# Kernel optimization log

Hardware: AMD Instinct MI355X
Metric: run time of the kernel (lower is better)

Reference implementation:

```python
import jax, jax.numpy as jnp
import numpy as np

MIN_BOX_SIZE = 0.05


def setup_inputs() -> dict:
    key = jax.random.key(0)
    mask_fg = jax.random.uniform(key, (256, 1, 512, 512), dtype=jnp.float32)
    return {"mask_fg": mask_fg}


def reference(mask_fg):
    # mask_fg: (B, 1, H, W). Returns boxes: (B, 4) as [x0, y0, x1, y1] in [0, 1].
    B, _, H, W = mask_fg.shape
    m = mask_fg[:, 0] > 0.5  # (B, H, W) boolean foreground mask

    row_any = jnp.any(m, axis=2)  # (B, H): row contains a foreground pixel
    col_any = jnp.any(m, axis=1)  # (B, W): col contains a foreground pixel
    empty = ~jnp.any(row_any, axis=1)  # (B,): no foreground at all

    ys = jnp.arange(H, dtype=jnp.float32)
    xs = jnp.arange(W, dtype=jnp.float32)

    # masked min/max of row / column indices, normalized (matches torch: idx / H, idx / W)
    y_min = jnp.min(jnp.where(row_any, ys, jnp.float32(H)), axis=1) / H
    y_max = jnp.max(jnp.where(row_any, ys, jnp.float32(-1)), axis=1) / H
    x_min = jnp.min(jnp.where(col_any, xs, jnp.float32(W)), axis=1) / W
    x_max = jnp.max(jnp.where(col_any, xs, jnp.float32(-1)), axis=1) / W

    s = jnp.float32(MIN_BOX_SIZE)

    def expand(lo, hi):
        too_small = (hi - lo) < s
        c = (lo + hi) * 0.5
        lo2 = jnp.maximum(jnp.float32(0.0), c - s * 0.5)
        hi2 = jnp.minimum(jnp.float32(1.0), c + s * 0.5)
        return jnp.where(too_small, lo2, lo), jnp.where(too_small, hi2, hi)

    x_min, x_max = expand(x_min, x_max)
    y_min, y_max = expand(y_min, y_max)

    boxes = jnp.stack([x_min, y_min, x_max, y_max], axis=1)  # (B, 4)
    default = jnp.array([0.25, 0.25, 0.75, 0.75], dtype=jnp.float32)
    boxes = jnp.where(empty[:, None], default[None, :], boxes)
    return boxes
```

## Files before the change

kernel.cpp:

```cpp
#include <hip/hip_runtime.h>


constexpr int H = 512;
constexpr int W = 512;
constexpr int THREADS = 512;
constexpr int NWAVE = THREADS / 64;
constexpr int BIG = 1 << 29;

__device__ __forceinline__ int block_min(int v, int t, int* s_tmp, int* s_res) {
    #pragma unroll
    for (int off = 32; off > 0; off >>= 1) v = min(v, __shfl_down(v, off));
    if ((t & 63) == 0) s_tmp[t >> 6] = v;
    __syncthreads();
    if (t == 0) {
        int m = s_tmp[0];
        #pragma unroll
        for (int w = 1; w < NWAVE; ++w) m = min(m, s_tmp[w]);
        *s_res = m;
    }
    __syncthreads();
    return *s_res;
}

__global__ __launch_bounds__(THREADS)
void scan_kernel(const float* __restrict__ mask, int* __restrict__ ws) {
    const int b = blockIdx.x;
    const int phase = blockIdx.y;
    const float4* __restrict__ img =
        reinterpret_cast<const float4*>(mask) + (size_t)b * (H * W / 4);
    const int t = threadIdx.x;
    __shared__ int s_tmp[NWAVE];
    __shared__ int s_res;

    int result = BIG;

    if (phase < 2) {
        const int rr = t >> 7;
        const int c4 = t & 127;
        for (int g = 0; g < H / 4; ++g) {
            const int gg = (phase == 0) ? g : (H / 4 - 1 - g);
            const int r = gg * 4 + rr;
            const float4 v = img[(r << 7) + c4];
            const bool fg = (v.x > 0.5f) || (v.y > 0.5f) ||
                            (v.z > 0.5f) || (v.w > 0.5f);
            const int key = fg ? (phase == 0 ? r : -r) : BIG;
            const int res = block_min(key, t, s_tmp, &s_res);
            if (res < BIG) { result = res; break; }
        }
    } else {
        const int r = t;
        for (int s = 0; s < W / 4; ++s) {
            const int ss = (phase == 2) ? s : (W / 4 - 1 - s);
            const float4 v = img[(r << 7) + ss];
            const int c = ss * 4;
            int key = BIG;
            if (phase == 2) {
                if (v.w > 0.5f) key = c + 3;
                if (v.z > 0.5f) key = c + 2;
                if (v.y > 0.5f) key = c + 1;
                if (v.x > 0.5f) key = c;
            } else {
                if (v.x > 0.5f) key = -c;
                if (v.y > 0.5f) key = -(c + 1);
                if (v.z > 0.5f) key = -(c + 2);
                if (v.w > 0.5f) key = -(c + 3);
            }
            const int res = block_min(key, t, s_tmp, &s_res);
            if (res < BIG) { result = res; break; }
        }
    }

    if (t == 0) ws[b * 4 + phase] = result;
}

__global__ __launch_bounds__(256)
void box_kernel(const int* __restrict__ ws, float* __restrict__ out, int B) {
    const int b = blockIdx.x * blockDim.x + threadIdx.x;
    if (b >= B) return;
    const int ymin = ws[b * 4 + 0];
    const int nymax = ws[b * 4 + 1];
    const int xmin = ws[b * 4 + 2];
    const int nxmax = ws[b * 4 + 3];
    float x0, y0, x1, y1;
    if (ymin >= BIG) {
        x0 = 0.25f; y0 = 0.25f; x1 = 0.75f; y1 = 0.75f;
    } else {
        const int ymax = -nymax, xmax = -nxmax;
        y0 = (float)ymin * (1.0f / H);
        y1 = (float)ymax * (1.0f / H);
        x0 = (float)xmin * (1.0f / W);
        x1 = (float)xmax * (1.0f / W);
        const float s = 0.05f;
        if (x1 - x0 < s) {
            const float c = (x0 + x1) * 0.5f;
            x0 = fmaxf(0.0f, c - s * 0.5f);
            x1 = fminf(1.0f, c + s * 0.5f);
        }
        if (y1 - y0 < s) {
            const float c = (y0 + y1) * 0.5f;
            y0 = fmaxf(0.0f, c - s * 0.5f);
            y1 = fminf(1.0f, c + s * 0.5f);
        }
    }
    reinterpret_cast<float4*>(out)[b] = make_float4(x0, y0, x1, y1);
}

extern "C" void kernel_launch(void* const* d_in, const int* in_sizes, int n_in,
                              void* d_out, int out_size, void* d_ws, size_t ws_size,
                              hipStream_t stream) {
    const float* mask = (const float*)d_in[0];
    float* out = (float*)d_out;
    int* ws = (int*)d_ws;
    const int B = in_sizes[0] / (H * W);
    dim3 grid(B, 4);
    scan_kernel<<<grid, THREADS, 0, stream>>>(mask, ws);
    box_kernel<<<(B + 255) / 256, 256, 0, stream>>>(ws, out, B);
}
```

Before: 301.9 us.

## Fuse scan and box kernels into one block per image with wave-level early exit

```diff
diff --git a/kernel.cpp b/kernel.cpp
--- a/kernel.cpp
+++ b/kernel.cpp
@@ -3,106 +3,94 @@
 
 constexpr int H = 512;
 constexpr int W = 512;
-constexpr int THREADS = 512;
-constexpr int NWAVE = THREADS / 64;
 constexpr int BIG = 1 << 29;
 
-__device__ __forceinline__ int block_min(int v, int t, int* s_tmp, int* s_res) {
+__device__ __forceinline__ int wave_min_bcast(int v) {
     #pragma unroll
     for (int off = 32; off > 0; off >>= 1) v = min(v, __shfl_down(v, off));
-    if ((t & 63) == 0) s_tmp[t >> 6] = v;
-    __syncthreads();
-    if (t == 0) {
-        int m = s_tmp[0];
-        #pragma unroll
-        for (int w = 1; w < NWAVE; ++w) m = min(m, s_tmp[w]);
-        *s_res = m;
-    }
-    __syncthreads();
-    return *s_res;
+    return __shfl(v, 0);
 }
 
-__global__ __launch_bounds__(THREADS)
-void scan_kernel(const float* __restrict__ mask, int* __restrict__ ws) {
+__global__ __launch_bounds__(256)
+void bbox_kernel(const float* __restrict__ mask, float* __restrict__ out) {
     const int b = blockIdx.x;
-    const int phase = blockIdx.y;
     const float4* __restrict__ img =
         reinterpret_cast<const float4*>(mask) + (size_t)b * (H * W / 4);
     const int t = threadIdx.x;
-    __shared__ int s_tmp[NWAVE];
-    __shared__ int s_res;
+    const int wave = t >> 6;
+    const int lane = t & 63;
+    __shared__ int s_res[4];
 
     int result = BIG;
 
-    if (phase < 2) {
-        const int rr = t >> 7;
-        const int c4 = t & 127;
-        for (int g = 0; g < H / 4; ++g) {
-            const int gg = (phase == 0) ? g : (H / 4 - 1 - g);
-            const int r = gg * 4 + rr;
-            const float4 v = img[(r << 7) + c4];
-            const bool fg = (v.x > 0.5f) || (v.y > 0.5f) ||
-                            (v.z > 0.5f) || (v.w > 0.5f);
-            const int key = fg ? (phase == 0 ? r : -r) : BIG;
-            const int res = block_min(key, t, s_tmp, &s_res);
-            if (res < BIG) { result = res; break; }
+    if (wave < 2) {
+        for (int i = 0; i < H; ++i) {
+            const int r = (wave == 0) ? i : (H - 1 - i);
+            const float4 a = img[(r << 7) + lane];
+            const float4 c = img[(r << 7) + 64 + lane];
+            const bool fg = (a.x > 0.5f) | (a.y > 0.5f) | (a.z > 0.5f) | (a.w > 0.5f) |
+                            (c.x > 0.5f) | (c.y > 0.5f) | (c.z > 0.5f) | (c.w > 0.5f);
+            if (__any(fg)) { result = (wave == 0) ? r : -r; break; }
         }
     } else {
-        const int r = t;
-        for (int s = 0; s < W / 4; ++s) {
-            const int ss = (phase == 2) ? s : (W / 4 - 1 - s);
-            const float4 v = img[(r << 7) + ss];
-            const int c = ss * 4;
+        for (int i = 0; i < W / 4; ++i) {
+            const int ss = (wave == 2) ? i : (W / 4 - 1 - i);
+            const int c = ss << 2;
             int key = BIG;
-            if (phase == 2) {
-                if (v.w > 0.5f) key = c + 3;
-                if (v.z > 0.5f) key = c + 2;
-                if (v.y > 0.5f) key = c + 1;
-                if (v.x > 0.5f) key = c;
-            } else {
-                if (v.x > 0.5f) key = -c;
-                if (v.y > 0.5f) key = -(c + 1);
-                if (v.z > 0.5f) key = -(c + 2);
-                if (v.w > 0.5f) key = -(c + 3);
+            #pragma unroll
+            for (int k = 0; k < 8; ++k) {
+                const int r = lane + (k << 6);
+                const float4 v = img[(r << 7) + ss];
+                int kk = BIG;
+                if (wave == 2) {
+                    if (v.w > 0.5f) kk = c + 3;
+                    if (v.z > 0.5f) kk = c + 2;
+                    if (v.y > 0.5f) kk = c + 1;
+                    if (v.x > 0.5f) kk = c;
+                } else {
+                    if (v.x > 0.5f) kk = -c;
+                    if (v.y > 0.5f) kk = -(c + 1);
+                    if (v.z > 0.5f) kk = -(c + 2);
+                    if (v.w > 0.5f) kk = -(c + 3);
+                }
+                key = min(key, kk);
             }
-            const int res = block_min(key, t, s_tmp, &s_res);
-            if (res < BIG) { result = res; break; }
+            key = wave_min_bcast(key);
+            if (key < BIG) { result = key; break; }
         }
     }
 
-    if (t == 0) ws[b * 4 + phase] = result;
-}
+    if (lane == 0) s_res[wave] = result;
+    __syncthreads();
 
-__global__ __launch_bounds__(256)
-void box_kernel(const int* __restrict__ ws, float* __restrict__ out, int B) {
-    const int b = blockIdx.x * blockDim.x + threadIdx.x;
-    if (b >= B) return;
-    const int ymin = ws[b * 4 + 0];
-    const int nymax = ws[b * 4 + 1];
-    const int xmin = ws[b * 4 + 2];
-    const int nxmax = ws[b * 4 + 3];
-    float x0, y0, x1, y1;
-    if (ymin >= BIG) {
-        x0 = 0.25f; y0 = 0.25f; x1 = 0.75f; y1 = 0.75f;
-    } else {
-        const int ymax = -nymax, xmax = -nxmax;
-        y0 = (float)ymin * (1.0f / H);
-        y1 = (float)ymax * (1.0f / H);
-        x0 = (float)xmin * (1.0f / W);
-        x1 = (float)xmax * (1.0f / W);
-        const float s = 0.05f;
-        if (x1 - x0 < s) {
-            const float c = (x0 + x1) * 0.5f;
-            x0 = fmaxf(0.0f, c - s * 0.5f);
-            x1 = fminf(1.0f, c + s * 0.5f);
+    if (t == 0) {
+        const int ymin  = s_res[0];
+        const int nymax = s_res[1];
+        const int xmin  = s_res[2];
+        const int nxmax = s_res[3];
+        float x0, y0, x1, y1;
+        if (ymin >= BIG) {
+            x0 = 0.25f; y0 = 0.25f; x1 = 0.75f; y1 = 0.75f;
+        } else {
+            const int ymax = -nymax, xmax = -nxmax;
+            y0 = (float)ymin * (1.0f / H);
+            y1 = (float)ymax * (1.0f / H);
+            x0 = (float)xmin * (1.0f / W);
+            x1 = (float)xmax * (1.0f / W);
+            const float s = 0.05f;
+            if (x1 - x0 < s) {
+                const float c = (x0 + x1) * 0.5f;
+                x0 = fmaxf(0.0f, c - s * 0.5f);
+                x1 = fminf(1.0f, c + s * 0.5f);
+            }
+            if (y1 - y0 < s) {
+                const float c = (y0 + y1) * 0.5f;
+                y0 = fmaxf(0.0f, c - s * 0.5f);
+                y1 = fminf(1.0f, c + s * 0.5f);
+            }
         }
-        if (y1 - y0 < s) {
-            const float c = (y0 + y1) * 0.5f;
-            y0 = fmaxf(0.0f, c - s * 0.5f);
-            y1 = fminf(1.0f, c + s * 0.5f);
-        }
+        reinterpret_cast<float4*>(out)[b] = make_float4(x0, y0, x1, y1);
     }
-    reinterpret_cast<float4*>(out)[b] = make_float4(x0, y0, x1, y1);
 }
 
 extern "C" void kernel_launch(void* const* d_in, const int* in_sizes, int n_in,
@@ -110,9 +98,6 @@
                               hipStream_t stream) {
     const float* mask = (const float*)d_in[0];
     float* out = (float*)d_out;
-    int* ws = (int*)d_ws;
     const int B = in_sizes[0] / (H * W);
-    dim3 grid(B, 4);
-    scan_kernel<<<grid, THREADS, 0, stream>>>(mask, ws);
-    box_kernel<<<(B + 255) / 256, 256, 0, stream>>>(ws, out, B);
+    bbox_kernel<<<B, 256, 0, stream>>>(mask, out);
 }
```

After: 296.7 us. About the same (-1.7%).
